# Performance work log

Measured on AMD Instinct MI355X. Metric: run time of the kernel, lower is better.

Reference implementation:

```python
import jax, jax.numpy as jnp
import numpy as np

B, S, D = 2, 2048, 1024
H, KS = 16, 64

def setup_inputs() -> dict:
    key = jax.random.key(0)
    k1, k2, k3, k4, k5 = jax.random.split(key, 5)
    return {
        "x": jax.random.normal(k1, (B, S, D), dtype=jnp.float32),
        "Wq": jax.random.normal(k2, (D, KS, H), dtype=jnp.float32) * 0.02,
        "Wk": jax.random.normal(k3, (D, KS, H), dtype=jnp.float32) * 0.02,
        "Wv": jax.random.normal(k4, (D, KS, H), dtype=jnp.float32) * 0.02,
        "kernel": jax.random.normal(k5, (H * KS, KS), dtype=jnp.float32) * 0.02,
    }

def reference(x, Wq, Wk, Wv, kernel):
    b, s, d = x.shape
    ks, h = Wq.shape[1], Wq.shape[2]
    # projections: heads-last layout [b, s, ks, h]
    q = jnp.einsum('bsd,dkh->bskh', x, Wq)
    k = jnp.einsum('bsd,dkh->bskh', x, Wk)
    v = jnp.einsum('bsd,dkh->bskh', x, Wv)
    # scores [b, i(query), l(key), h]
    scores = jnp.einsum('bikh,blkh->bilh', q, k) / jnp.sqrt(jnp.float32(ks))
    # strictly-upper-triangular (future) mask, as in the original:
    # band_part(ones,0,-1) - eye  ->  1 where l > i
    li = jnp.arange(s)
    mask = (li[None, :] > li[:, None]).astype(jnp.float32)  # [s, s]
    scores = scores - 1e8 * mask[None, :, :, None]
    weights = jax.nn.softmax(scores, axis=2)  # softmax over key axis l
    heads = jnp.einsum('bilh,blkh->bikh', weights, v)  # [b, s, ks, h]
    heads = heads.reshape(b, s, ks * h)  # row-major flatten of (ks, h), matching tf.reshape
    return heads @ kernel  # [b, s, ks]
```

## Files before the change

kernel.cpp:

```cpp
#include <hip/hip_runtime.h>
#include <hip/hip_bf16.h>

#define BB 2
#define SS 2048
#define DD 1024
#define HH 16
#define KSZ 64

typedef __attribute__((ext_vector_type(8))) short s16x8;
typedef __attribute__((ext_vector_type(4))) float f32x4;
typedef __attribute__((ext_vector_type(8))) unsigned short u16x8;
typedef __attribute__((ext_vector_type(4))) unsigned short u16x4;
typedef __attribute__((ext_vector_type(2))) unsigned int u32x2;
typedef unsigned short u16;

__device__ __forceinline__ u16 bf16rne(float f) {
  unsigned int u = __float_as_uint(f);
  unsigned int r = (u + 0x7FFFu + ((u >> 16) & 1u)) >> 16;
  return (u16)r;
}

__device__ __forceinline__ void lds_dma16(const u16* g, u16* l) {
  __builtin_amdgcn_global_load_lds(
      (const __attribute__((address_space(1))) unsigned int*)(const void*)g,
      (__attribute__((address_space(3))) unsigned int*)(void*)l, 16, 0, 0);
}

__global__ __launch_bounds__(256) void prep_all(
    const float* __restrict__ x, const float* __restrict__ Wq,
    const float* __restrict__ Wk, const float* __restrict__ Wv,
    const float* __restrict__ kern, u16* __restrict__ xb,
    u16* __restrict__ Wt, u16* __restrict__ BpT) {
  __shared__ float Ts[64][65];
  const int bid = blockIdx.x;
  const int tid = threadIdx.x;
  if (bid < 2048) {
    int idx = (bid * 256 + tid) * 8;
    float4 a = *(const float4*)(x + idx);
    float4 b = *(const float4*)(x + idx + 4);
    u16x8 v;
    v[0] = bf16rne(a.x); v[1] = bf16rne(a.y); v[2] = bf16rne(a.z); v[3] = bf16rne(a.w);
    v[4] = bf16rne(b.x); v[5] = bf16rne(b.y); v[6] = bf16rne(b.z); v[7] = bf16rne(b.w);
    *(u16x8*)(xb + idx) = v;
  } else if (bid < 2816) {
    const int bx = bid - 2048;
    const int p = bx >> 8, rem = bx & 255;
    const int d0 = (rem & 15) * 64, n0 = (rem >> 4) * 64;
    const float* W = (p == 0) ? Wq : (p == 1) ? Wk : Wv;
    u16* Wo = Wt + (size_t)p * DD * DD;
    #pragma unroll
    for (int i = 0; i < 4; ++i) {
      int f4 = tid + i * 256;
      int r = f4 >> 4, c4 = f4 & 15;
      float4 v = *(const float4*)(W + (size_t)(d0 + r) * DD + n0 + c4 * 4);
      Ts[r][c4 * 4 + 0] = v.x; Ts[r][c4 * 4 + 1] = v.y;
      Ts[r][c4 * 4 + 2] = v.z; Ts[r][c4 * 4 + 3] = v.w;
    }
    __syncthreads();
    #pragma unroll
    for (int i = 0; i < 4; ++i) {
      int ch = tid + i * 256;
      int n = ch >> 4, d4 = ch & 15;
      u16x4 o;
      #pragma unroll
      for (int j = 0; j < 4; ++j) o[j] = bf16rne(Ts[d4 * 4 + j][n]);
      *(u16x4*)(Wo + (size_t)(n0 + n) * DD + d0 + d4 * 4) = o;
    }
  } else {
    const int n = bid - 2816;
    const int k4 = tid * 4;
    u16x4 o;
    #pragma unroll
    for (int j = 0; j < 4; ++j) {
      int kp = k4 + j;
      int h = kp >> 6, k = kp & 63;
      o[j] = bf16rne(kern[(size_t)(k * HH + h) * KSZ + n]);
    }
    *(u16x4*)(BpT + (size_t)n * (HH * KSZ) + k4) = o;
  }
}

__global__ __launch_bounds__(256) void proj_kernel(
    const u16* __restrict__ xb, const u16* __restrict__ Wt,
    u16* __restrict__ qkvT) {
  const int xcd = blockIdx.x & 7;
  const int idx = blockIdx.x >> 3;
  const int mt = (xcd >> 1) * 8 + (idx & 7);
  const int nt = (xcd & 1) * 4 + ((idx >> 3) & 3);
  const int p  = idx >> 5;
  const int m0 = mt * 128, n0 = nt * 128;
  const u16* W = Wt + (size_t)p * DD * DD;
  u16* outp = qkvT + (size_t)p * (BB * HH * SS * KSZ);

  __shared__ __align__(16) unsigned char raw[34816];
  u16* As0 = (u16*)raw;
  u16* Bs0 = As0 + 128 * 32;
  u16* As1 = Bs0 + 128 * 32;
  u16* Bs1 = As1 + 128 * 32;
  u16* Cs  = (u16*)raw;

  const int tid = threadIdx.x;
  const int wave = tid >> 6, lane = tid & 63;
  const int g = lane >> 4, c = lane & 15;
  const int mbase = (wave & 1) * 64, nbase = (wave >> 1) * 64;

  const int lr = lane >> 2, lc = lane & 3;
  const int swz = (lc ^ ((lr >> 1) & 3)) * 8;
  const int rA0 = (wave * 2 + 0) * 16;
  const int rA1 = (wave * 2 + 1) * 16;
  const u16* srcA0 = xb + (size_t)(m0 + rA0 + lr) * DD + swz;
  const u16* srcA1 = xb + (size_t)(m0 + rA1 + lr) * DD + swz;
  const u16* srcB0 = W  + (size_t)(n0 + rA0 + lr) * DD + swz;
  const u16* srcB1 = W  + (size_t)(n0 + rA1 + lr) * DD + swz;
  const int sl0 = rA0 * 32, sl1 = rA1 * 32;

  f32x4 acc[4][4];
  #pragma unroll
  for (int i = 0; i < 4; ++i)
    #pragma unroll
    for (int j = 0; j < 4; ++j) acc[i][j] = {0.f, 0.f, 0.f, 0.f};

  lds_dma16(srcA0, As0 + sl0);  lds_dma16(srcA1, As0 + sl1);
  lds_dma16(srcB0, Bs0 + sl0);  lds_dma16(srcB1, Bs0 + sl1);
  __syncthreads();

  const int jsw = (c >> 1) & 3;
  #pragma unroll 2
  for (int t = 0; t < 32; ++t) {
    u16* Ac = (t & 1) ? As1 : As0;
    u16* Bc = (t & 1) ? Bs1 : Bs0;
    if (t < 31) {
      u16* An = (t & 1) ? As0 : As1;
      u16* Bn = (t & 1) ? Bs0 : Bs1;
      const int ko = (t + 1) * 32;
      lds_dma16(srcA0 + ko, An + sl0);  lds_dma16(srcA1 + ko, An + sl1);
      lds_dma16(srcB0 + ko, Bn + sl0);  lds_dma16(srcB1 + ko, Bn + sl1);
    }
    s16x8 af[4], bfr[4];
    #pragma unroll
    for (int mf = 0; mf < 4; ++mf)
      af[mf] = *(const s16x8*)&Ac[(mbase + mf * 16 + c) * 32 + ((g ^ jsw) * 8)];
    #pragma unroll
    for (int nf = 0; nf < 4; ++nf)
      bfr[nf] = *(const s16x8*)&Bc[(nbase + nf * 16 + c) * 32 + ((g ^ jsw) * 8)];
    #pragma unroll
    for (int mf = 0; mf < 4; ++mf)
      #pragma unroll
      for (int nf = 0; nf < 4; ++nf)
        acc[mf][nf] = __builtin_amdgcn_mfma_f32_16x16x32_bf16(
            af[mf], bfr[nf], acc[mf][nf], 0, 0, 0);
    __syncthreads();
  }

  const float cscale = (p == 0) ? 0.125f * 1.44269504f : 1.0f;
  #pragma unroll
  for (int mf = 0; mf < 4; ++mf)
    #pragma unroll
    for (int nf = 0; nf < 4; ++nf)
      #pragma unroll
      for (int r = 0; r < 4; ++r)
        Cs[(mbase + mf * 16 + g * 4 + r) * 136 + nbase + nf * 16 + c] =
            bf16rne(acc[mf][nf][r] * cscale);
  __syncthreads();
  const int b = m0 >> 11;
  if (p < 2) {
    int hh = tid >> 4, si = tid & 15;
    #pragma unroll
    for (int i = 0; i < 8; ++i) {
      int row = i * 16 + si;
      int s = (m0 + row) & 2047;
      u16x8 v;
      #pragma unroll
      for (int kp = 0; kp < 8; ++kp) v[kp] = Cs[row * 136 + kp * 16 + hh];
      *(u16x8*)(outp + ((size_t)(b * HH + hh) * SS + s) * KSZ + (n0 >> 4)) = v;
    }
  } else {
    const int s0 = m0 & 2047;
    #pragma unroll
    for (int i = 0; i < 8; ++i) {
      int chunk = tid + i * 256;
      int colid = chunk >> 4;
      int hh = colid >> 3, kp = colid & 7;
      int s8 = chunk & 15;
      u16x8 v;
      #pragma unroll
      for (int j = 0; j < 8; ++j) v[j] = Cs[(s8 * 8 + j) * 136 + kp * 16 + hh];
      *(u16x8*)(outp + ((size_t)(b * HH + hh) * KSZ + (n0 >> 4) + kp) * SS +
                s0 + s8 * 8) = v;
    }
  }
}

__global__ __launch_bounds__(512) void attn_kernel(
    const u16* __restrict__ qkvT, u16* __restrict__ headsB) {
  const int bid = blockIdx.x;
  const int hb = bid & 31;
  const int uu = bid >> 5;
  const int p  = (uu < 8) ? uu : 23 - uu;
  const int itB = 2 * p + 1;
  const int h = hb & 15, b = hb >> 4;
  const size_t plane = (size_t)(b * HH + h) * SS * KSZ;
  const size_t PSZ = (size_t)BB * HH * SS * KSZ;
  const u16* Qg = qkvT + plane;
  const u16* Kg = qkvT + PSZ + plane;
  const u16* Vg = qkvT + 2 * PSZ + plane;

  __shared__ u16 Ks[2][64 * 64];
  __shared__ u16 Vt[2][64 * 64];
  __shared__ u16 Ps[128 * 64];

  const int tid = threadIdx.x;
  const int wave = tid >> 6, lane = tid & 63;
  const int g = lane >> 4, c = lane & 15;
  const int wq0 = (wave & 3) * 16;
  const int myIt = itB - ((wave < 4) ? 1 : 0);
  const int pq0 = wave * 16;
  const int sr = tid >> 3, sc = tid & 7;
  const int so = sr * 64 + ((sc ^ (sr & 7)) * 8);

  s16x8 bq0 = *(const s16x8*)(Qg + (size_t)(myIt * 64 + wq0 + c) * KSZ + g * 8);
  s16x8 bq1 = *(const s16x8*)(Qg + (size_t)(myIt * 64 + wq0 + c) * KSZ + 32 + g * 8);

  u16x8 kr = *(const u16x8*)(Kg + (size_t)sr * KSZ + sc * 8);
  u16x8 vr = *(const u16x8*)(Vg + (size_t)sr * SS + sc * 8);
  *(u16x8*)&Ks[0][so] = kr;
  *(u16x8*)&Vt[0][so] = vr;
  if (itB >= 1) {
    kr = *(const u16x8*)(Kg + (size_t)(64 + sr) * KSZ + sc * 8);
    vr = *(const u16x8*)(Vg + (size_t)sr * SS + 64 + sc * 8);
  }
  __syncthreads();

  f32x4 o[4];
  #pragma unroll
  for (int mf = 0; mf < 4; ++mf) o[mf] = {0.f, 0.f, 0.f, 0.f};
  float l_i = 0.f;
  const int cswz = c & 7;

  #pragma unroll 1
  for (int t = 0; t <= itB; ++t) {
    const int buf = t & 1;
    if (t < itB) {
      const int nb = buf ^ 1;
      *(u16x8*)&Ks[nb][so] = kr;
      *(u16x8*)&Vt[nb][so] = vr;
      if (t + 2 <= itB) {
        const int kv2 = t + 2;
        kr = *(const u16x8*)(Kg + (size_t)(kv2 * 64 + sr) * KSZ + sc * 8);
        vr = *(const u16x8*)(Vg + (size_t)sr * SS + kv2 * 64 + sc * 8);
      }
    }
    if (t <= myIt) {
      f32x4 s[4];
      #pragma unroll
      for (int mf = 0; mf < 4; ++mf) s[mf] = {0.f, 0.f, 0.f, 0.f};
      #pragma unroll
      for (int ks = 0; ks < 2; ++ks) {
        const s16x8 bq = ks ? bq1 : bq0;
        #pragma unroll
        for (int mf = 0; mf < 4; ++mf) {
          s16x8 ak = *(const s16x8*)&Ks[buf][(mf * 16 + c) * 64 +
                                            (((ks * 4 + g) ^ cswz) * 8)];
          s[mf] = __builtin_amdgcn_mfma_f32_16x16x32_bf16(ak, bq, s[mf], 0, 0, 0);
        }
      }
      if (t == myIt) {
        const int qloc = wq0 + c;
        #pragma unroll
        for (int mf = 0; mf < 4; ++mf)
          #pragma unroll
          for (int r = 0; r < 4; ++r)
            if (mf * 16 + g * 4 + r > qloc) s[mf][r] = -1e30f;
      }
      float ps = 0.f;
      #pragma unroll
      for (int mf = 0; mf < 4; ++mf) {
        float p0 = __builtin_amdgcn_exp2f(s[mf][0]);
        float p1 = __builtin_amdgcn_exp2f(s[mf][1]);
        float p2 = __builtin_amdgcn_exp2f(s[mf][2]);
        float p3 = __builtin_amdgcn_exp2f(s[mf][3]);
        ps += (p0 + p1) + (p2 + p3);
        u32x2 d;
        d[0] = (__float_as_uint(p0) >> 16) | (__float_as_uint(p1) & 0xFFFF0000u);
        d[1] = (__float_as_uint(p2) >> 16) | (__float_as_uint(p3) & 0xFFFF0000u);
        *(u32x2*)&Ps[(pq0 + c) * 64 + (((mf * 2 + (g >> 1)) ^ cswz) * 8) +
                     ((g & 1) * 4)] = d;
      }
      l_i += ps;
      #pragma unroll
      for (int ks = 0; ks < 2; ++ks) {
        s16x8 bp = *(const s16x8*)&Ps[(pq0 + c) * 64 +
                                      (((ks * 4 + g) ^ cswz) * 8)];
        #pragma unroll
        for (int mf = 0; mf < 4; ++mf) {
          s16x8 av = *(const s16x8*)&Vt[buf][(mf * 16 + c) * 64 +
                                             (((ks * 4 + g) ^ cswz) * 8)];
          o[mf] = __builtin_amdgcn_mfma_f32_16x16x32_bf16(av, bp, o[mf], 0, 0, 0);
        }
      }
    }
    __syncthreads();
  }
  l_i += __shfl_xor(l_i, 16);
  l_i += __shfl_xor(l_i, 32);
  const float inv = 1.0f / l_i;
  const int q = myIt * 64 + wq0 + c;
  #pragma unroll
  for (int mf = 0; mf < 4; ++mf) {
    u16x4 hv;
    #pragma unroll
    for (int r = 0; r < 4; ++r) hv[r] = bf16rne(o[mf][r] * inv);
    *(u16x4*)(headsB + plane + (size_t)q * KSZ + mf * 16 + g * 4) = hv;
  }
}

__global__ __launch_bounds__(256) void out_kernel(
    const u16* __restrict__ headsB, const u16* __restrict__ BpT,
    float* __restrict__ out) {
  const int m0 = blockIdx.x * 16;
  const int tid = threadIdx.x;
  const int wave = tid >> 6, lane = tid & 63;
  const int g = lane >> 4, c = lane & 15;

  const int m = m0 + c;
  const int b = m >> 11, s = m & 2047;

  f32x4 acc[4];
  #pragma unroll
  for (int nf = 0; nf < 4; ++nf) acc[nf] = {0.f, 0.f, 0.f, 0.f};

  #pragma unroll
  for (int it = 0; it < 8; ++it) {
    const int kb = wave * 256 + it * 32;
    const int hh = kb >> 6, kk = (kb & 63) + g * 8;
    s16x8 a = *(const s16x8*)(headsB +
        ((size_t)(b * HH + hh) * SS + s) * KSZ + kk);
    #pragma unroll
    for (int nf = 0; nf < 4; ++nf) {
      s16x8 bf = *(const s16x8*)(BpT +
          (size_t)(nf * 16 + c) * (HH * KSZ) + kb + g * 8);
      acc[nf] = __builtin_amdgcn_mfma_f32_16x16x32_bf16(a, bf, acc[nf], 0, 0, 0);
    }
  }

  __shared__ __align__(16) float red[4][64][16];
  #pragma unroll
  for (int nf = 0; nf < 4; ++nf)
    *(f32x4*)&red[wave][lane][nf * 4] = acc[nf];
  __syncthreads();

  const int mi = tid >> 4, n4 = (tid & 15) * 4;
  const int gg = mi >> 2, rr = mi & 3;
  float4 res;
  float* rp = &res.x;
  #pragma unroll
  for (int j = 0; j < 4; ++j) {
    int n = n4 + j;
    int cc = n & 15, nf = n >> 4;
    rp[j] = red[0][gg * 16 + cc][nf * 4 + rr] + red[1][gg * 16 + cc][nf * 4 + rr] +
            red[2][gg * 16 + cc][nf * 4 + rr] + red[3][gg * 16 + cc][nf * 4 + rr];
  }
  *(float4*)(out + (size_t)(m0 + mi) * KSZ + n4) = res;
}

extern "C" void kernel_launch(void* const* d_in, const int* in_sizes, int n_in,
                              void* d_out, int out_size, void* d_ws, size_t ws_size,
                              hipStream_t stream) {
  const float* x    = (const float*)d_in[0];
  const float* Wq   = (const float*)d_in[1];
  const float* Wk   = (const float*)d_in[2];
  const float* Wv   = (const float*)d_in[3];
  const float* kern = (const float*)d_in[4];
  float* out = (float*)d_out;

  u16* xb     = (u16*)d_ws;
  u16* Wt     = xb + (size_t)4096 * 1024;
  u16* qkvT   = Wt + (size_t)3 * 1024 * 1024;
  u16* headsB = qkvT + (size_t)3 * BB * HH * SS * KSZ;
  u16* BpT    = headsB + (size_t)BB * HH * SS * KSZ;

  prep_all<<<dim3(2880), 256, 0, stream>>>(x, Wq, Wk, Wv, kern, xb, Wt, BpT);
  proj_kernel<<<dim3(768), 256, 0, stream>>>(xb, Wt, qkvT);
  attn_kernel<<<dim3(512), 512, 0, stream>>>(qkvT, headsB);
  out_kernel<<<dim3(256), 256, 0, stream>>>(headsB, BpT, out);
}
```

Baseline: 162.1 us.

## Replace LDS DMA loads with register-staged global loads in QKV GEMM

The projection GEMM no longer fills its double-buffered LDS tiles with direct global-to-LDS DMA (global_load_lds). Each thread now loads 16-byte chunks into registers two k-steps ahead and writes them to the next LDS buffer while the current one is consumed. The aim is deeper prefetch and better latency hiding, with the XOR swizzle computed per row. In exchange it uses more VGPRs and adds explicit LDS write instructions that compete with the MFMA stream.

```diff
diff --git a/kernel.cpp b/kernel.cpp
--- a/kernel.cpp
+++ b/kernel.cpp
@@ -18,12 +18,6 @@
   unsigned int u = __float_as_uint(f);
   unsigned int r = (u + 0x7FFFu + ((u >> 16) & 1u)) >> 16;
   return (u16)r;
-}
-
-__device__ __forceinline__ void lds_dma16(const u16* g, u16* l) {
-  __builtin_amdgcn_global_load_lds(
-      (const __attribute__((address_space(1))) unsigned int*)(const void*)g,
-      (__attribute__((address_space(3))) unsigned int*)(void*)l, 16, 0, 0);
 }
 
 __global__ __launch_bounds__(256) void prep_all(
@@ -104,15 +98,16 @@
   const int g = lane >> 4, c = lane & 15;
   const int mbase = (wave & 1) * 64, nbase = (wave >> 1) * 64;
 
-  const int lr = lane >> 2, lc = lane & 3;
-  const int swz = (lc ^ ((lr >> 1) & 3)) * 8;
-  const int rA0 = (wave * 2 + 0) * 16;
-  const int rA1 = (wave * 2 + 1) * 16;
-  const u16* srcA0 = xb + (size_t)(m0 + rA0 + lr) * DD + swz;
-  const u16* srcA1 = xb + (size_t)(m0 + rA1 + lr) * DD + swz;
-  const u16* srcB0 = W  + (size_t)(n0 + rA0 + lr) * DD + swz;
-  const u16* srcB1 = W  + (size_t)(n0 + rA1 + lr) * DD + swz;
-  const int sl0 = rA0 * 32, sl1 = rA1 * 32;
+  const int row0 = tid >> 2, sc0 = tid & 3;
+  const int row1 = row0 + 64;
+  const int so0 = (sc0 ^ ((row0 >> 1) & 3)) * 8;
+  const int so1 = (sc0 ^ ((row1 >> 1) & 3)) * 8;
+  const u16* srcA0 = xb + (size_t)(m0 + row0) * DD + so0;
+  const u16* srcA1 = xb + (size_t)(m0 + row1) * DD + so1;
+  const u16* srcB0 = W  + (size_t)(n0 + row0) * DD + so0;
+  const u16* srcB1 = W  + (size_t)(n0 + row1) * DD + so1;
+  const int d0 = row0 * 32 + sc0 * 8;
+  const int d1 = row1 * 32 + sc0 * 8;
 
   f32x4 acc[4][4];
   #pragma unroll
@@ -120,8 +115,16 @@
     #pragma unroll
     for (int j = 0; j < 4; ++j) acc[i][j] = {0.f, 0.f, 0.f, 0.f};
 
-  lds_dma16(srcA0, As0 + sl0);  lds_dma16(srcA1, As0 + sl1);
-  lds_dma16(srcB0, Bs0 + sl0);  lds_dma16(srcB1, Bs0 + sl1);
+  u16x8 ra0 = *(const u16x8*)srcA0;
+  u16x8 ra1 = *(const u16x8*)srcA1;
+  u16x8 rb0 = *(const u16x8*)srcB0;
+  u16x8 rb1 = *(const u16x8*)srcB1;
+  *(u16x8*)&As0[d0] = ra0;  *(u16x8*)&As0[d1] = ra1;
+  *(u16x8*)&Bs0[d0] = rb0;  *(u16x8*)&Bs0[d1] = rb1;
+  ra0 = *(const u16x8*)(srcA0 + 32);
+  ra1 = *(const u16x8*)(srcA1 + 32);
+  rb0 = *(const u16x8*)(srcB0 + 32);
+  rb1 = *(const u16x8*)(srcB1 + 32);
   __syncthreads();
 
   const int jsw = (c >> 1) & 3;
@@ -132,9 +135,15 @@
     if (t < 31) {
       u16* An = (t & 1) ? As0 : As1;
       u16* Bn = (t & 1) ? Bs0 : Bs1;
-      const int ko = (t + 1) * 32;
-      lds_dma16(srcA0 + ko, An + sl0);  lds_dma16(srcA1 + ko, An + sl1);
-      lds_dma16(srcB0 + ko, Bn + sl0);  lds_dma16(srcB1 + ko, Bn + sl1);
+      *(u16x8*)&An[d0] = ra0;  *(u16x8*)&An[d1] = ra1;
+      *(u16x8*)&Bn[d0] = rb0;  *(u16x8*)&Bn[d1] = rb1;
+      if (t < 30) {
+        const int ko = (t + 2) * 32;
+        ra0 = *(const u16x8*)(srcA0 + ko);
+        ra1 = *(const u16x8*)(srcA1 + ko);
+        rb0 = *(const u16x8*)(srcB0 + ko);
+        rb1 = *(const u16x8*)(srcB1 + ko);
+      }
     }
     s16x8 af[4], bfr[4];
     #pragma unroll
```

Measured after the change: 162.6 us. Within noise of the previous version (+0.3%).
